# Kernel optimization log

Hardware: AMD Instinct MI355X
Metric: run time of the kernel (lower is better)

The kernel has to match this reference:

```python
import jax, jax.numpy as jnp
import numpy as np

B, C, H, W = 2, 256, 64, 64
NUM_HEADS = 4
HEAD_DIM = C // NUM_HEADS
N = H * W


def setup_inputs() -> dict:
    key = jax.random.key(0)
    ks = jax.random.split(key, 10)
    x = jax.random.normal(ks[0], (B, C, H, W), dtype=jnp.float32)
    # mostly-True mask; diagonal forced True so every row has a valid key
    m = jax.random.uniform(ks[1], (B, N, N)) > 0.1
    spatial_mask = m | jnp.eye(N, dtype=bool)[None]
    s = 1.0 / np.sqrt(C)
    wq = jax.random.normal(ks[2], (C, C), dtype=jnp.float32) * s
    bq = jnp.zeros((C,), jnp.float32)
    wk = jax.random.normal(ks[3], (C, C), dtype=jnp.float32) * s
    bk = jnp.zeros((C,), jnp.float32)
    wv = jax.random.normal(ks[4], (C, C), dtype=jnp.float32) * s
    bv = jnp.zeros((C,), jnp.float32)
    # torch zero-inits out_proj; use random weights for a non-trivial baseline
    wo = jax.random.normal(ks[5], (C, C), dtype=jnp.float32) * s
    bo = jnp.zeros((C,), jnp.float32)
    return {"x": x, "spatial_mask": spatial_mask, "wq": wq, "bq": bq,
            "wk": wk, "bk": bk, "wv": wv, "bv": bv, "wo": wo, "bo": bo}


def reference(x, spatial_mask, wq, bq, wk, bk, wv, bv, wo, bo):
    b, c, h, w = x.shape
    n = h * w
    nh, hd = NUM_HEADS, HEAD_DIM
    scale = hd ** -0.5
    x_flat = x.reshape(b, c, n).transpose(0, 2, 1)           # [b, n, c]
    q = (x_flat @ wq.T + bq).reshape(b, n, nh, hd).transpose(0, 2, 1, 3)
    k = (x_flat @ wk.T + bk).reshape(b, n, nh, hd).transpose(0, 2, 1, 3)
    v = (x_flat @ wv.T + bv).reshape(b, n, nh, hd).transpose(0, 2, 1, 3)
    logits = jnp.einsum('bhqd,bhkd->bhqk', q, k) * scale      # [b, nh, n, n]
    logits = jnp.where(spatial_mask[:, None], logits, -jnp.inf)
    attn = jax.nn.softmax(logits, axis=-1)                    # dropout = identity (eval)
    out = jnp.einsum('bhqk,bhkd->bhqd', attn, v)              # [b, nh, n, hd]
    out = out.transpose(0, 2, 1, 3).reshape(b, n, c)
    out = out @ wo.T + bo
    return out.transpose(0, 2, 1).reshape(b, c, h, w)
```

## Files before the change

### kernel.cpp

```cpp
#include <hip/hip_runtime.h>
#include <math.h>

namespace {
constexpr int B_    = 2;
constexpr int C_    = 256;
constexpr int NHEAD = 4;
constexpr int HDIM  = 64;
constexpr int NTOK  = 4096;
constexpr float SCALE = 0.125f;
constexpr float LOG2E = 1.44269504f;
}

typedef _Float16 half8  __attribute__((ext_vector_type(8)));
typedef _Float16 half4  __attribute__((ext_vector_type(4)));
typedef float    floatx4 __attribute__((ext_vector_type(4)));

__global__ __launch_bounds__(256) void pack_mask(
    const unsigned int* __restrict__ m32, unsigned int* __restrict__ packed)
{
    int c0 = 0, c1 = 0, c2 = 0, c3 = 0;
    #pragma unroll
    for (int i = 0; i < 16; i++) {
        const unsigned int d = m32[i];
        c0 += (d == 0x00000001u);
        c1 += (d == 0x3F803F80u);
        c2 += (d == 0x3F800000u);
        c3 += (d == 0x01010101u);
    }
    int fmt = 1, best = c1;
    if (c0 > best) { best = c0; fmt = 0; }
    if (c2 > best) { best = c2; fmt = 2; }
    if (c3 > best) { best = c3; fmt = 3; }

    const unsigned int W = blockIdx.x * 256 + threadIdx.x;
    unsigned int bits = 0;
    if (fmt == 1) {
        const uint4* p4 = (const uint4*)(m32 + (size_t)W * 16);
        #pragma unroll
        for (int i = 0; i < 4; i++) {
            const uint4 v = p4[i];
            const unsigned int d[4] = { v.x, v.y, v.z, v.w };
            #pragma unroll
            for (int j = 0; j < 4; j++) {
                const int e = i * 8 + j * 2;
                bits |= ((d[j] & 0xFFFFu) ? 1u : 0u) << e;
                bits |= ((d[j] >> 16)     ? 1u : 0u) << (e + 1);
            }
        }
    } else if (fmt != 3) {
        const uint4* p4 = (const uint4*)(m32 + (size_t)W * 32);
        #pragma unroll
        for (int i = 0; i < 8; i++) {
            const uint4 v = p4[i];
            bits |= (v.x ? 1u : 0u) << (i * 4 + 0);
            bits |= (v.y ? 1u : 0u) << (i * 4 + 1);
            bits |= (v.z ? 1u : 0u) << (i * 4 + 2);
            bits |= (v.w ? 1u : 0u) << (i * 4 + 3);
        }
    } else {
        const uint4* p4 = (const uint4*)(m32 + (size_t)W * 8);
        #pragma unroll
        for (int i = 0; i < 2; i++) {
            const uint4 v = p4[i];
            const unsigned int d[4] = { v.x, v.y, v.z, v.w };
            #pragma unroll
            for (int j = 0; j < 4; j++) {
                const int e = (i * 4 + j) * 4;
                bits |= ((d[j] & 0x000000FFu) ? 1u : 0u) << (e + 0);
                bits |= ((d[j] & 0x0000FF00u) ? 1u : 0u) << (e + 1);
                bits |= ((d[j] & 0x00FF0000u) ? 1u : 0u) << (e + 2);
                bits |= ((d[j] & 0xFF000000u) ? 1u : 0u) << (e + 3);
            }
        }
    }
    packed[W] = bits;
}

__global__ __launch_bounds__(256) void transpose_x(
    const float* __restrict__ x, _Float16* __restrict__ xT)
{
    const int nt = blockIdx.x;
    const int ct = blockIdx.y;
    const int b  = blockIdx.z;
    const int t  = threadIdx.x;
    const int n0 = nt * 64, c0 = ct * 64;

    __shared__ _Float16 tx[64 * 72];

    const int cr = t >> 4;
    const int nu = (t & 15) * 4;
    #pragma unroll
    for (int pass = 0; pass < 4; pass++) {
        const int c = c0 + pass * 16 + cr;
        const float4 v = *(const float4*)&x[((size_t)b * C_ + c) * NTOK + n0 + nu];
        tx[(nu + 0) * 72 + pass * 16 + cr] = (_Float16)v.x;
        tx[(nu + 1) * 72 + pass * 16 + cr] = (_Float16)v.y;
        tx[(nu + 2) * 72 + pass * 16 + cr] = (_Float16)v.z;
        tx[(nu + 3) * 72 + pass * 16 + cr] = (_Float16)v.w;
    }
    __syncthreads();
    const int row = t >> 2;
    const int sc  = (t & 3) * 16;
    const half8 o0 = *(const half8*)&tx[row * 72 + sc];
    const half8 o1 = *(const half8*)&tx[row * 72 + sc + 8];
    _Float16* dst = xT + ((size_t)b * NTOK + n0 + row) * C_ + c0 + sc;
    *(half8*)&dst[0] = o0;
    *(half8*)&dst[8] = o1;
}

__global__ __launch_bounds__(256) void qkv_mfma(
    const _Float16* __restrict__ xT,
    const float* __restrict__ wq, const float* __restrict__ bq,
    const float* __restrict__ wk, const float* __restrict__ bk,
    const float* __restrict__ wv, const float* __restrict__ bv,
    _Float16* __restrict__ qo, _Float16* __restrict__ ko,
    _Float16* __restrict__ vo)
{
    const int nt = blockIdx.x;
    const int h  = blockIdx.y;
    const int b  = blockIdx.z / 3;
    const int p  = blockIdx.z % 3;

    const float* w; const float* bias;
    if (p == 0)      { w = wq; bias = bq; }
    else if (p == 1) { w = wk; bias = bk; }
    else             { w = wv; bias = bv; }

    const int t    = threadIdx.x;
    const int wid  = t >> 6;
    const int lane = t & 63;
    const int quad = lane >> 4;
    const int l15  = lane & 15;
    const int n0  = nt * 64;
    const int co0 = h * 64;

    __shared__ _Float16 wsh[64 * 72];
    __shared__ _Float16 xsh[64 * 72];
    __shared__ _Float16 tbuf[64 * 72];

    const int srow = t >> 2;
    const int sc   = (t & 3) * 16;

    floatx4 acc[4];
    #pragma unroll
    for (int i = 0; i < 4; i++) acc[i] = (floatx4)0.f;

    const _Float16* xTb = xT + ((size_t)b * NTOK + n0) * C_;

    for (int c0 = 0; c0 < C_; c0 += 64) {
        {
            const float* wr = &w[(size_t)(co0 + srow) * C_ + c0 + sc];
            half8 h0, h1;
            #pragma unroll
            for (int u = 0; u < 2; u++) {
                const float4 a = *(const float4*)&wr[u * 4];
                h0[u*4+0]=(_Float16)a.x; h0[u*4+1]=(_Float16)a.y;
                h0[u*4+2]=(_Float16)a.z; h0[u*4+3]=(_Float16)a.w;
            }
            #pragma unroll
            for (int u = 0; u < 2; u++) {
                const float4 a = *(const float4*)&wr[8 + u * 4];
                h1[u*4+0]=(_Float16)a.x; h1[u*4+1]=(_Float16)a.y;
                h1[u*4+2]=(_Float16)a.z; h1[u*4+3]=(_Float16)a.w;
            }
            *(half8*)&wsh[srow * 72 + sc]     = h0;
            *(half8*)&wsh[srow * 72 + sc + 8] = h1;
        }
        {
            const _Float16* xr = &xTb[(size_t)srow * C_ + c0 + sc];
            *(half8*)&xsh[srow * 72 + sc]     = *(const half8*)&xr[0];
            *(half8*)&xsh[srow * 72 + sc + 8] = *(const half8*)&xr[8];
        }
        __syncthreads();
        const half8 a0 = *(const half8*)&wsh[(wid * 16 + l15) * 72 + quad * 8];
        const half8 a1 = *(const half8*)&wsh[(wid * 16 + l15) * 72 + 32 + quad * 8];
        #pragma unroll
        for (int nt2 = 0; nt2 < 4; nt2++) {
            const half8 b0 = *(const half8*)&xsh[(nt2 * 16 + l15) * 72 + quad * 8];
            const half8 b1 = *(const half8*)&xsh[(nt2 * 16 + l15) * 72 + 32 + quad * 8];
            acc[nt2] = __builtin_amdgcn_mfma_f32_16x16x32_f16(a0, b0, acc[nt2], 0, 0, 0);
            acc[nt2] = __builtin_amdgcn_mfma_f32_16x16x32_f16(a1, b1, acc[nt2], 0, 0, 0);
        }
        __syncthreads();
    }

    const float4 bb4 = *(const float4*)&bias[co0 + wid * 16 + quad * 4];
    const float bb[4] = { bb4.x, bb4.y, bb4.z, bb4.w };

    if (p < 2) {
        const float osc = (p == 0) ? (SCALE * LOG2E) : 1.0f;
        #pragma unroll
        for (int nt2 = 0; nt2 < 4; nt2++) {
            half4 hv;
            #pragma unroll
            for (int i = 0; i < 4; i++)
                hv[i] = (_Float16)((acc[nt2][i] + bb[i]) * osc);
            *(half4*)&tbuf[(nt2 * 16 + l15) * 72 + wid * 16 + quad * 4] = hv;
        }
        __syncthreads();
        _Float16* dh = (p == 0 ? qo : ko) + (size_t)(b * NHEAD + h) * NTOK * HDIM;
        const half8 o0 = *(const half8*)&tbuf[srow * 72 + sc];
        const half8 o1 = *(const half8*)&tbuf[srow * 72 + sc + 8];
        *(half8*)&dh[(size_t)(n0 + srow) * HDIM + sc]     = o0;
        *(half8*)&dh[(size_t)(n0 + srow) * HDIM + sc + 8] = o1;
    } else {
        #pragma unroll
        for (int nt2 = 0; nt2 < 4; nt2++)
            #pragma unroll
            for (int i = 0; i < 4; i++)
                tbuf[(wid * 16 + quad * 4 + i) * 72 + nt2 * 16 + l15] =
                    (_Float16)(acc[nt2][i] + bb[i]);
        __syncthreads();
        _Float16* vth = vo + (size_t)(b * NHEAD + h) * HDIM * NTOK;
        const half8 o0 = *(const half8*)&tbuf[srow * 72 + sc];
        const half8 o1 = *(const half8*)&tbuf[srow * 72 + sc + 8];
        *(half8*)&vth[(size_t)srow * NTOK + n0 + sc]     = o0;
        *(half8*)&vth[(size_t)srow * NTOK + n0 + sc + 8] = o1;
    }
}

__global__ __launch_bounds__(256) void attn(
    const _Float16* __restrict__ q, const _Float16* __restrict__ k,
    const _Float16* __restrict__ vt, const unsigned int* __restrict__ mpacked,
    _Float16* __restrict__ ao)
{
    const int b  = blockIdx.z;
    const int h  = blockIdx.y;
    const int q0 = blockIdx.x * 64;
    const int t    = threadIdx.x;
    const int w    = t >> 6;
    const int lane = t & 63;
    const int quad = lane >> 4;
    const int l15  = lane & 15;

    __shared__ _Float16 ks[2][64 * 72];
    __shared__ _Float16 vs[2][64 * 72];
    __shared__ _Float16 ps[64 * 72];
    __shared__ float bcast[64];

    const size_t head_off = (size_t)(b * NHEAD + h) * NTOK * HDIM;
    const _Float16* qb  = q  + head_off;
    const _Float16* kb  = k  + head_off;
    const _Float16* vtb = vt + head_off;
    const unsigned int* mrow = mpacked + (size_t)b * NTOK * 128;

    const int qrow = q0 + w * 16 + l15;
    half8 aq0 = *(const half8*)&qb[(size_t)qrow * HDIM + quad * 8];
    half8 aq1 = *(const half8*)&qb[(size_t)qrow * HDIM + 32 + quad * 8];

    const int srow = t >> 2;
    const int scol = (t & 3) * 16;

    half8 kreg0 = *(const half8*)&kb[(size_t)srow * HDIM + scol];
    half8 kreg1 = *(const half8*)&kb[(size_t)srow * HDIM + scol + 8];
    half8 vreg0 = *(const half8*)&vtb[(size_t)srow * NTOK + scol];
    half8 vreg1 = *(const half8*)&vtb[(size_t)srow * NTOK + scol + 8];

    float l_i[4] = { 0.f, 0.f, 0.f, 0.f };
    floatx4 o_acc[4];
    #pragma unroll
    for (int i = 0; i < 4; i++) o_acc[i] = (floatx4)0.f;

    for (int kt = 0; kt < NTOK / 64; kt++) {
        const int k0 = kt * 64;
        _Float16* ksc = ks[kt & 1];
        _Float16* vsc = vs[kt & 1];
        *(half8*)&ksc[srow * 72 + scol]     = kreg0;
        *(half8*)&ksc[srow * 72 + scol + 8] = kreg1;
        *(half8*)&vsc[srow * 72 + scol]     = vreg0;
        *(half8*)&vsc[srow * 72 + scol + 8] = vreg1;
        __syncthreads();

        if (kt + 1 < NTOK / 64) {
            kreg0 = *(const half8*)&kb[(size_t)(k0 + 64 + srow) * HDIM + scol];
            kreg1 = *(const half8*)&kb[(size_t)(k0 + 64 + srow) * HDIM + scol + 8];
            vreg0 = *(const half8*)&vtb[(size_t)srow * NTOK + k0 + 64 + scol];
            vreg1 = *(const half8*)&vtb[(size_t)srow * NTOK + k0 + 64 + scol + 8];
        }
        uint2 mw[4];
        #pragma unroll
        for (int i = 0; i < 4; i++)
            mw[i] = *(const uint2*)&mrow[(size_t)(q0 + w * 16 + quad * 4 + i) * 128 + (k0 >> 5)];

        floatx4 sa[4];
        #pragma unroll
        for (int ct = 0; ct < 4; ct++) {
            sa[ct] = (floatx4)0.f;
            const half8 b0 = *(const half8*)&ksc[(ct * 16 + l15) * 72 + quad * 8];
            const half8 b1 = *(const half8*)&ksc[(ct * 16 + l15) * 72 + 32 + quad * 8];
            sa[ct] = __builtin_amdgcn_mfma_f32_16x16x32_f16(aq0, b0, sa[ct], 0, 0, 0);
            sa[ct] = __builtin_amdgcn_mfma_f32_16x16x32_f16(aq1, b1, sa[ct], 0, 0, 0);
        }

        #pragma unroll
        for (int ct = 0; ct < 4; ct++) {
            #pragma unroll
            for (int i = 0; i < 4; i++) {
                const unsigned int word = (ct < 2) ? mw[i].x : mw[i].y;
                const bool keep = (word >> (((ct & 1) << 4) + l15)) & 1u;
                const float v = keep ? sa[ct][i] : -3.0e38f;
                const float p = exp2f(fminf(v, 15.f));
                l_i[i] += p;
                ps[(w * 16 + quad * 4 + i) * 72 + ct * 16 + l15] = (_Float16)p;
            }
        }

        const half8 pb0 = *(const half8*)&ps[(w * 16 + l15) * 72 + quad * 8];
        const half8 pb1 = *(const half8*)&ps[(w * 16 + l15) * 72 + 32 + quad * 8];
        #pragma unroll
        for (int dt = 0; dt < 4; dt++) {
            const half8 va0 = *(const half8*)&vsc[(dt * 16 + l15) * 72 + quad * 8];
            const half8 va1 = *(const half8*)&vsc[(dt * 16 + l15) * 72 + 32 + quad * 8];
            o_acc[dt] = __builtin_amdgcn_mfma_f32_16x16x32_f16(va0, pb0, o_acc[dt], 0, 0, 0);
            o_acc[dt] = __builtin_amdgcn_mfma_f32_16x16x32_f16(va1, pb1, o_acc[dt], 0, 0, 0);
        }
    }

    #pragma unroll
    for (int i = 0; i < 4; i++)
        #pragma unroll
        for (int off = 1; off < 16; off <<= 1)
            l_i[i] += __shfl_xor(l_i[i], off, 64);

    if (l15 == 0) {
        floatx4 lv; lv[0] = l_i[0]; lv[1] = l_i[1]; lv[2] = l_i[2]; lv[3] = l_i[3];
        *(floatx4*)&bcast[w * 16 + quad * 4] = lv;
    }
    const float lf  = bcast[w * 16 + l15];
    const float inv = (lf > 0.f) ? (1.0f / lf) : 0.f;

    _Float16* aob = ao + ((size_t)b * NTOK + q0 + w * 16 + l15) * C_ + h * 64;
    #pragma unroll
    for (int dt = 0; dt < 4; dt++) {
        half4 r;
        #pragma unroll
        for (int rr = 0; rr < 4; rr++) r[rr] = (_Float16)(o_acc[dt][rr] * inv);
        *(half4*)&aob[dt * 16 + quad * 4] = r;
    }
}

__global__ __launch_bounds__(256) void out_mfma(
    const _Float16* __restrict__ ao, const float* __restrict__ wo,
    const float* __restrict__ bo, float* __restrict__ out)
{
    const int nt  = blockIdx.x;
    const int cot = blockIdx.y;
    const int b   = blockIdx.z;
    const int t    = threadIdx.x;
    const int wid  = t >> 6;
    const int lane = t & 63;
    const int quad = lane >> 4;
    const int l15  = lane & 15;
    const int n0  = nt * 64;
    const int co0 = cot * 64;

    __shared__ _Float16 wsh[64 * 72];
    __shared__ _Float16 ash[64 * 72];
    __shared__ float    tf[64 * 68];

    const int srow = t >> 2;
    const int sc   = (t & 3) * 16;

    floatx4 acc[4];
    #pragma unroll
    for (int i = 0; i < 4; i++) acc[i] = (floatx4)0.f;

    const _Float16* aob = ao + ((size_t)b * NTOK + n0) * C_;

    for (int c0 = 0; c0 < C_; c0 += 64) {
        {
            const float* wr = &wo[(size_t)(co0 + srow) * C_ + c0 + sc];
            half8 h0, h1;
            #pragma unroll
            for (int u = 0; u < 2; u++) {
                const float4 a = *(const float4*)&wr[u * 4];
                h0[u*4+0]=(_Float16)a.x; h0[u*4+1]=(_Float16)a.y;
                h0[u*4+2]=(_Float16)a.z; h0[u*4+3]=(_Float16)a.w;
            }
            #pragma unroll
            for (int u = 0; u < 2; u++) {
                const float4 a = *(const float4*)&wr[8 + u * 4];
                h1[u*4+0]=(_Float16)a.x; h1[u*4+1]=(_Float16)a.y;
                h1[u*4+2]=(_Float16)a.z; h1[u*4+3]=(_Float16)a.w;
            }
            *(half8*)&wsh[srow * 72 + sc]     = h0;
            *(half8*)&wsh[srow * 72 + sc + 8] = h1;
        }
        {
            const _Float16* ar = &aob[(size_t)srow * C_ + c0 + sc];
            *(half8*)&ash[srow * 72 + sc]     = *(const half8*)&ar[0];
            *(half8*)&ash[srow * 72 + sc + 8] = *(const half8*)&ar[8];
        }
        __syncthreads();
        const half8 a0 = *(const half8*)&wsh[(wid * 16 + l15) * 72 + quad * 8];
        const half8 a1 = *(const half8*)&wsh[(wid * 16 + l15) * 72 + 32 + quad * 8];
        #pragma unroll
        for (int nt2 = 0; nt2 < 4; nt2++) {
            const half8 b0 = *(const half8*)&ash[(nt2 * 16 + l15) * 72 + quad * 8];
            const half8 b1 = *(const half8*)&ash[(nt2 * 16 + l15) * 72 + 32 + quad * 8];
            acc[nt2] = __builtin_amdgcn_mfma_f32_16x16x32_f16(a0, b0, acc[nt2], 0, 0, 0);
            acc[nt2] = __builtin_amdgcn_mfma_f32_16x16x32_f16(a1, b1, acc[nt2], 0, 0, 0);
        }
        __syncthreads();
    }

    #pragma unroll
    for (int nt2 = 0; nt2 < 4; nt2++)
        #pragma unroll
        for (int i = 0; i < 4; i++)
            tf[(wid * 16 + quad * 4 + i) * 68 + nt2 * 16 + l15] = acc[nt2][i];
    __syncthreads();

    const int row = t >> 2;
    const int c4  = (t & 3) * 16;
    const float bb = bo[co0 + row];
    float* orow = &out[((size_t)(b * C_ + co0 + row)) * NTOK + n0 + c4];
    #pragma unroll
    for (int u = 0; u < 4; u++) {
        float4 v = *(const float4*)&tf[row * 68 + c4 + u * 4];
        v.x += bb; v.y += bb; v.z += bb; v.w += bb;
        *(float4*)&orow[u * 4] = v;
    }
}

extern "C" void kernel_launch(void* const* d_in, const int* in_sizes, int n_in,
                              void* d_out, int out_size, void* d_ws, size_t ws_size,
                              hipStream_t stream) {
    const float* x    = (const float*)d_in[0];
    const void*  mask = d_in[1];
    const float* wq   = (const float*)d_in[2];
    const float* bq   = (const float*)d_in[3];
    const float* wk   = (const float*)d_in[4];
    const float* bk   = (const float*)d_in[5];
    const float* wv   = (const float*)d_in[6];
    const float* bv   = (const float*)d_in[7];
    const float* wo   = (const float*)d_in[8];
    const float* bo   = (const float*)d_in[9];
    float* out = (float*)d_out;

    const size_t qkv_elems = (size_t)B_ * NHEAD * NTOK * HDIM;
    _Float16* wsh = (_Float16*)d_ws;
    _Float16* qbuf  = wsh;
    _Float16* kbuf  = wsh + qkv_elems;
    _Float16* vtbuf = wsh + 2 * qkv_elems;
    _Float16* xt_ao = wsh + 3 * qkv_elems;
    unsigned int* mpacked = (unsigned int*)(wsh + 4 * qkv_elems);

    pack_mask<<<dim3((B_ * NTOK * 128) / 256), 256, 0, stream>>>(
        (const unsigned int*)mask, mpacked);
    transpose_x<<<dim3(NTOK / 64, C_ / 64, B_), 256, 0, stream>>>(x, xt_ao);
    qkv_mfma<<<dim3(NTOK / 64, NHEAD, B_ * 3), 256, 0, stream>>>(
        xt_ao, wq, bq, wk, bk, wv, bv, qbuf, kbuf, vtbuf);
    attn<<<dim3(NTOK / 64, NHEAD, B_), 256, 0, stream>>>(
        qbuf, kbuf, vtbuf, mpacked, xt_ao);
    out_mfma<<<dim3(NTOK / 64, C_ / 64, B_), 256, 0, stream>>>(
        xt_ao, wo, bo, out);
}
```

Measured before the change: 339.7 us.

## Fuse x transpose into QKV projection and transpose S tile in attention

Removes the separate transpose_x kernel: the QKV projection now reads fp32 x directly, converts it to fp16 and transposes it while staging into shared memory. In the attention kernel the QK^T MFMA operands are swapped, so each lane holds one query row. That lets it load a single mask uint2 per tile instead of four, write P as a vectorised half4, and reduce the row sum with two shuffles instead of a shuffle tree plus a shared-memory broadcast. The cost is that each QKV block re-reads and re-converts fp32 x for every head and projection, adding global traffic.

```diff
diff --git a/kernel.cpp b/kernel.cpp
--- a/kernel.cpp
+++ b/kernel.cpp
@@ -76,40 +76,8 @@
     packed[W] = bits;
 }
 
-__global__ __launch_bounds__(256) void transpose_x(
-    const float* __restrict__ x, _Float16* __restrict__ xT)
-{
-    const int nt = blockIdx.x;
-    const int ct = blockIdx.y;
-    const int b  = blockIdx.z;
-    const int t  = threadIdx.x;
-    const int n0 = nt * 64, c0 = ct * 64;
-
-    __shared__ _Float16 tx[64 * 72];
-
-    const int cr = t >> 4;
-    const int nu = (t & 15) * 4;
-    #pragma unroll
-    for (int pass = 0; pass < 4; pass++) {
-        const int c = c0 + pass * 16 + cr;
-        const float4 v = *(const float4*)&x[((size_t)b * C_ + c) * NTOK + n0 + nu];
-        tx[(nu + 0) * 72 + pass * 16 + cr] = (_Float16)v.x;
-        tx[(nu + 1) * 72 + pass * 16 + cr] = (_Float16)v.y;
-        tx[(nu + 2) * 72 + pass * 16 + cr] = (_Float16)v.z;
-        tx[(nu + 3) * 72 + pass * 16 + cr] = (_Float16)v.w;
-    }
-    __syncthreads();
-    const int row = t >> 2;
-    const int sc  = (t & 3) * 16;
-    const half8 o0 = *(const half8*)&tx[row * 72 + sc];
-    const half8 o1 = *(const half8*)&tx[row * 72 + sc + 8];
-    _Float16* dst = xT + ((size_t)b * NTOK + n0 + row) * C_ + c0 + sc;
-    *(half8*)&dst[0] = o0;
-    *(half8*)&dst[8] = o1;
-}
-
 __global__ __launch_bounds__(256) void qkv_mfma(
-    const _Float16* __restrict__ xT,
+    const float* __restrict__ x,
     const float* __restrict__ wq, const float* __restrict__ bq,
     const float* __restrict__ wk, const float* __restrict__ bk,
     const float* __restrict__ wv, const float* __restrict__ bv,
@@ -140,12 +108,14 @@
 
     const int srow = t >> 2;
     const int sc   = (t & 3) * 16;
+    const int cr   = t >> 4;
+    const int nu   = (t & 15) * 4;
 
     floatx4 acc[4];
     #pragma unroll
     for (int i = 0; i < 4; i++) acc[i] = (floatx4)0.f;
 
-    const _Float16* xTb = xT + ((size_t)b * NTOK + n0) * C_;
+    const float* xb = x + (size_t)b * C_ * NTOK;
 
     for (int c0 = 0; c0 < C_; c0 += 64) {
         {
@@ -167,9 +137,15 @@
             *(half8*)&wsh[srow * 72 + sc + 8] = h1;
         }
         {
-            const _Float16* xr = &xTb[(size_t)srow * C_ + c0 + sc];
-            *(half8*)&xsh[srow * 72 + sc]     = *(const half8*)&xr[0];
-            *(half8*)&xsh[srow * 72 + sc + 8] = *(const half8*)&xr[8];
+            #pragma unroll
+            for (int pass = 0; pass < 4; pass++) {
+                const int cl = pass * 16 + cr;
+                const float4 v = *(const float4*)&xb[(size_t)(c0 + cl) * NTOK + n0 + nu];
+                xsh[(nu + 0) * 72 + cl] = (_Float16)v.x;
+                xsh[(nu + 1) * 72 + cl] = (_Float16)v.y;
+                xsh[(nu + 2) * 72 + cl] = (_Float16)v.z;
+                xsh[(nu + 3) * 72 + cl] = (_Float16)v.w;
+            }
         }
         __syncthreads();
         const half8 a0 = *(const half8*)&wsh[(wid * 16 + l15) * 72 + quad * 8];
@@ -236,7 +212,6 @@
     __shared__ _Float16 ks[2][64 * 72];
     __shared__ _Float16 vs[2][64 * 72];
     __shared__ _Float16 ps[64 * 72];
-    __shared__ float bcast[64];
 
     const size_t head_off = (size_t)(b * NHEAD + h) * NTOK * HDIM;
     const _Float16* qb  = q  + head_off;
@@ -247,6 +222,7 @@
     const int qrow = q0 + w * 16 + l15;
     half8 aq0 = *(const half8*)&qb[(size_t)qrow * HDIM + quad * 8];
     half8 aq1 = *(const half8*)&qb[(size_t)qrow * HDIM + 32 + quad * 8];
+    const unsigned int* mq = &mrow[(size_t)qrow * 128];
 
     const int srow = t >> 2;
     const int scol = (t & 3) * 16;
@@ -256,7 +232,7 @@
     half8 vreg0 = *(const half8*)&vtb[(size_t)srow * NTOK + scol];
     half8 vreg1 = *(const half8*)&vtb[(size_t)srow * NTOK + scol + 8];
 
-    float l_i[4] = { 0.f, 0.f, 0.f, 0.f };
+    float l_loc = 0.f;
     floatx4 o_acc[4];
     #pragma unroll
     for (int i = 0; i < 4; i++) o_acc[i] = (floatx4)0.f;
@@ -277,32 +253,31 @@
             vreg0 = *(const half8*)&vtb[(size_t)srow * NTOK + k0 + 64 + scol];
             vreg1 = *(const half8*)&vtb[(size_t)srow * NTOK + k0 + 64 + scol + 8];
         }
-        uint2 mw[4];
-        #pragma unroll
-        for (int i = 0; i < 4; i++)
-            mw[i] = *(const uint2*)&mrow[(size_t)(q0 + w * 16 + quad * 4 + i) * 128 + (k0 >> 5)];
+        const uint2 mw = *(const uint2*)&mq[k0 >> 5];
 
         floatx4 sa[4];
         #pragma unroll
         for (int ct = 0; ct < 4; ct++) {
             sa[ct] = (floatx4)0.f;
-            const half8 b0 = *(const half8*)&ksc[(ct * 16 + l15) * 72 + quad * 8];
-            const half8 b1 = *(const half8*)&ksc[(ct * 16 + l15) * 72 + 32 + quad * 8];
-            sa[ct] = __builtin_amdgcn_mfma_f32_16x16x32_f16(aq0, b0, sa[ct], 0, 0, 0);
-            sa[ct] = __builtin_amdgcn_mfma_f32_16x16x32_f16(aq1, b1, sa[ct], 0, 0, 0);
+            const half8 ka0 = *(const half8*)&ksc[(ct * 16 + l15) * 72 + quad * 8];
+            const half8 ka1 = *(const half8*)&ksc[(ct * 16 + l15) * 72 + 32 + quad * 8];
+            sa[ct] = __builtin_amdgcn_mfma_f32_16x16x32_f16(ka0, aq0, sa[ct], 0, 0, 0);
+            sa[ct] = __builtin_amdgcn_mfma_f32_16x16x32_f16(ka1, aq1, sa[ct], 0, 0, 0);
         }
 
         #pragma unroll
         for (int ct = 0; ct < 4; ct++) {
+            const unsigned int word = (ct < 2) ? mw.x : mw.y;
+            const unsigned nib = (word >> (((ct & 1) << 4) + quad * 4)) & 0xFu;
+            half4 pv;
             #pragma unroll
             for (int i = 0; i < 4; i++) {
-                const unsigned int word = (ct < 2) ? mw[i].x : mw[i].y;
-                const bool keep = (word >> (((ct & 1) << 4) + l15)) & 1u;
-                const float v = keep ? sa[ct][i] : -3.0e38f;
+                const float v = ((nib >> i) & 1u) ? sa[ct][i] : -3.0e38f;
                 const float p = exp2f(fminf(v, 15.f));
-                l_i[i] += p;
-                ps[(w * 16 + quad * 4 + i) * 72 + ct * 16 + l15] = (_Float16)p;
-            }
+                l_loc += p;
+                pv[i] = (_Float16)p;
+            }
+            *(half4*)&ps[(w * 16 + l15) * 72 + ct * 16 + quad * 4] = pv;
         }
 
         const half8 pb0 = *(const half8*)&ps[(w * 16 + l15) * 72 + quad * 8];
@@ -316,18 +291,9 @@
         }
     }
 
-    #pragma unroll
-    for (int i = 0; i < 4; i++)
-        #pragma unroll
-        for (int off = 1; off < 16; off <<= 1)
-            l_i[i] += __shfl_xor(l_i[i], off, 64);
-
-    if (l15 == 0) {
-        floatx4 lv; lv[0] = l_i[0]; lv[1] = l_i[1]; lv[2] = l_i[2]; lv[3] = l_i[3];
-        *(floatx4*)&bcast[w * 16 + quad * 4] = lv;
-    }
-    const float lf  = bcast[w * 16 + l15];
-    const float inv = (lf > 0.f) ? (1.0f / lf) : 0.f;
+    l_loc += __shfl_xor(l_loc, 16, 64);
+    l_loc += __shfl_xor(l_loc, 32, 64);
+    const float inv = (l_loc > 0.f) ? (1.0f / l_loc) : 0.f;
 
     _Float16* aob = ao + ((size_t)b * NTOK + q0 + w * 16 + l15) * C_ + h * 64;
     #pragma unroll
@@ -443,16 +409,15 @@
     _Float16* qbuf  = wsh;
     _Float16* kbuf  = wsh + qkv_elems;
     _Float16* vtbuf = wsh + 2 * qkv_elems;
-    _Float16* xt_ao = wsh + 3 * qkv_elems;
+    _Float16* aobuf = wsh + 3 * qkv_elems;
     unsigned int* mpacked = (unsigned int*)(wsh + 4 * qkv_elems);
 
     pack_mask<<<dim3((B_ * NTOK * 128) / 256), 256, 0, stream>>>(
         (const unsigned int*)mask, mpacked);
-    transpose_x<<<dim3(NTOK / 64, C_ / 64, B_), 256, 0, stream>>>(x, xt_ao);
     qkv_mfma<<<dim3(NTOK / 64, NHEAD, B_ * 3), 256, 0, stream>>>(
-        xt_ao, wq, bq, wk, bk, wv, bv, qbuf, kbuf, vtbuf);
+        x, wq, bq, wk, bk, wv, bv, qbuf, kbuf, vtbuf);
     attn<<<dim3(NTOK / 64, NHEAD, B_), 256, 0, stream>>>(
-        qbuf, kbuf, vtbuf, mpacked, xt_ao);
+        qbuf, kbuf, vtbuf, mpacked, aobuf);
     out_mfma<<<dim3(NTOK / 64, C_ / 64, B_), 256, 0, stream>>>(
-        xt_ao, wo, bo, out);
-}
+        aobuf, wo, bo, out);
+}
```

New measurement: 331.0 us. -2.6%, faster.
